# Kernel optimization log

Measured on AMD Instinct MI355X. Metric: run time of the kernel, lower is better.

Reference implementation:

```python
import jax, jax.numpy as jnp
import numpy as np


def _lstm(x, Wih, Whh, bih, bhh):
    # x: [B, T, D_in]; PyTorch gate order: i, f, g, o. Returns all hidden states [B, T, H].
    B = x.shape[0]
    H = Whh.shape[1]
    b = bih + bhh  # [4H]
    xs = jnp.transpose(x, (1, 0, 2))  # [T, B, D_in] for scan over time

    def step(carry, xt):
        h, c = carry
        gates = xt @ Wih.T + h @ Whh.T + b  # [B, 4H]
        i, f, g, o = jnp.split(gates, 4, axis=-1)
        i = jax.nn.sigmoid(i)
        f = jax.nn.sigmoid(f)
        g = jnp.tanh(g)
        o = jax.nn.sigmoid(o)
        c = f * c + i * g
        h = o * jnp.tanh(c)
        return (h, c), h

    h0 = jnp.zeros((B, H), dtype=x.dtype)
    c0 = jnp.zeros((B, H), dtype=x.dtype)
    _, hs = jax.lax.scan(step, (h0, c0), xs)  # hs: [T, B, H]
    return jnp.transpose(hs, (1, 0, 2))  # [B, T, H]


def setup_inputs() -> dict:
    key = jax.random.key(0)
    ks = jax.random.split(key, 11)
    B, T, D_IN, H1, H2, NC = 256, 2048, 16, 5, 50, 20

    def u(k, shape, fan):
        bound = 1.0 / np.sqrt(fan)
        return jax.random.uniform(k, shape, jnp.float32, -bound, bound)

    x = jax.random.normal(ks[0], (B, T, D_IN), dtype=jnp.float32)
    return {
        "x": x,
        "W1ih": u(ks[1], (4 * H1, D_IN), H1),
        "W1hh": u(ks[2], (4 * H1, H1), H1),
        "b1ih": u(ks[3], (4 * H1,), H1),
        "b1hh": u(ks[4], (4 * H1,), H1),
        "W2ih": u(ks[5], (4 * H2, H1), H2),
        "W2hh": u(ks[6], (4 * H2, H2), H2),
        "b2ih": u(ks[7], (4 * H2,), H2),
        "b2hh": u(ks[8], (4 * H2,), H2),
        "Wfc": u(ks[9], (NC, H2), H2),
        "bfc": u(ks[10], (NC,), H2),
    }


def reference(x, W1ih, W1hh, b1ih, b1hh, W2ih, W2hh, b2ih, b2hh, Wfc, bfc):
    h1 = _lstm(x, W1ih, W1hh, b1ih, b1hh)      # [B, T, 5]
    h2 = _lstm(h1, W2ih, W2hh, b2ih, b2hh)     # [B, T, 50]
    # Dropout(p=0.2) in eval mode == identity (deterministic reference)
    last = h2[:, -1, :]                        # [B, 50]
    result = last @ Wfc.T + bfc                # [B, num_classes]
    return (result, last)
```

## Files before the change

kernel.cpp:

```cpp
#include <hip/hip_runtime.h>
#include <math.h>

namespace {

constexpr int TSEQ   = 2048;
constexpr int DIN    = 16;
constexpr int NH1    = 5;
constexpr int NH2    = 50;
constexpr int NCLS   = 20;
constexpr int CHUNK  = 64;
constexpr int NCHUNK = TSEQ / CHUNK;
constexpr int BATCH  = 256;
constexpr int GSTR   = 80;
constexpr int PROW   = 4 * GSTR;

__device__ __forceinline__ float fast_sigm(float x) {
    return __fdividef(1.f, 1.f + __expf(-x));
}
__device__ __forceinline__ float fast_tanh(float x) {
    return fmaf(2.f, fast_sigm(2.f * x), -1.f);
}

template <int CTRL>
__device__ __forceinline__ float qperm(float v) {
    int i = __builtin_bit_cast(int, v);
    int r = __builtin_amdgcn_update_dpp(i, i, CTRL, 0xf, 0xf, false);
    return __builtin_bit_cast(float, r);
}
__device__ __forceinline__ float rdlane(float v, int lane) {
    return __builtin_bit_cast(float,
        __builtin_amdgcn_readlane(__builtin_bit_cast(int, v), lane));
}

#define W4_BARRIER() asm volatile("s_waitcnt lgkmcnt(0)\n\ts_barrier" ::: "memory")

template <int N> struct IC { static constexpr int v = N; };

__global__ __launch_bounds__(320, 1) void lstm_fused_kernel(
    const float* __restrict__ x,
    const float* __restrict__ W1ih,
    const float* __restrict__ W1hh,
    const float* __restrict__ b1ih,
    const float* __restrict__ b1hh,
    const float* __restrict__ W2ih,
    const float* __restrict__ W2hh,
    const float* __restrict__ b2ih,
    const float* __restrict__ b2hh,
    const float* __restrict__ Wfc,
    const float* __restrict__ bfc,
    float* __restrict__ out)
{
    const int b    = blockIdx.x;
    const int tid  = threadIdx.x;
    const int lane = tid & 63;
    const int wv   = tid >> 6;

    __shared__ __align__(16) float s_x[2][CHUNK * DIN];
    __shared__ __align__(16) float s_part[2][4][PROW];
    __shared__ __align__(16) float s_h1[2][CHUNK][8];
    __shared__ float s_h2[NH2];

    const float* xb = x + (size_t)b * TSEQ * DIN;

    if (wv == 4) {
        const int r1 = (lane < NCLS) ? ((lane & 3) * NH1 + (lane >> 2)) : 0;
        float w1h[NH1], w1x[DIN];
        #pragma unroll
        for (int j = 0; j < NH1; ++j) w1h[j] = W1hh[r1 * NH1 + j];
        #pragma unroll
        for (int d = 0; d < DIN; ++d) w1x[d] = W1ih[r1 * DIN + d];
        const float bias1 = b1ih[r1] + b1hh[r1];
        const bool  isg1  = ((lane & 3) == 2) && (lane < NCLS);
        const float isc1  = isg1 ? 2.f : 1.f;
        const float osc1  = isg1 ? 2.f : 1.f;
        const float off1  = isg1 ? -1.f : 0.f;
        float c1 = 0.f;
        float sh0v = 0.f, sh1v = 0.f, sh2v = 0.f, sh3v = 0.f, sh4v = 0.f;
        float4 xr0, xr1, xr2, xr3;

        auto l1_prod = [&](const float* xs, float* h1out) {
            float4 xv0 = *(const float4*)(xs + 0);
            float4 xv1 = *(const float4*)(xs + 4);
            float4 xv2 = *(const float4*)(xs + 8);
            float4 xv3 = *(const float4*)(xs + 12);
            float sa = fmaf(xv0.y, w1x[1],  xv0.x * w1x[0]);
            sa = fmaf(xv0.z, w1x[2], sa);  sa = fmaf(xv0.w, w1x[3], sa);
            float sb = fmaf(xv1.y, w1x[5],  xv1.x * w1x[4]);
            sb = fmaf(xv1.z, w1x[6], sb);  sb = fmaf(xv1.w, w1x[7], sb);
            float sc = fmaf(xv2.y, w1x[9],  xv2.x * w1x[8]);
            sc = fmaf(xv2.z, w1x[10], sc); sc = fmaf(xv2.w, w1x[11], sc);
            float sd = fmaf(xv3.y, w1x[13], xv3.x * w1x[12]);
            sd = fmaf(xv3.z, w1x[14], sd); sd = fmaf(xv3.w, w1x[15], sd);
            float ha = fmaf(sh1v, w1h[1], sh0v * w1h[0]);
            ha = fmaf(sh2v, w1h[2], ha);
            float hb = fmaf(sh4v, w1h[4], sh3v * w1h[3]);
            float g1 = ((sa + sb) + (sc + sd)) + ((ha + hb) + bias1);
            float act = fmaf(osc1, fast_sigm(isc1 * g1), off1);
            float f_ = qperm<0xB1>(act);
            float gg = qperm<0x4E>(act);
            float o_ = qperm<0x1B>(act);
            c1 = fmaf(f_, c1, act * gg);
            float h1me = o_ * fast_tanh(c1);
            sh0v = rdlane(h1me, 0);  sh1v = rdlane(h1me, 4);
            sh2v = rdlane(h1me, 8);  sh3v = rdlane(h1me, 12);
            sh4v = rdlane(h1me, 16);
            if ((lane & 3) == 0 && lane < NCLS) h1out[lane >> 2] = h1me;
        };

        xr0 = ((const float4*)(xb))[lane];
        xr1 = ((const float4*)(xb + 256))[lane];
        xr2 = ((const float4*)(xb + 512))[lane];
        xr3 = ((const float4*)(xb + 768))[lane];
        ((float4*)s_x[0])[lane]       = xr0;
        ((float4*)s_x[0])[64 + lane]  = xr1;
        ((float4*)s_x[0])[128 + lane] = xr2;
        ((float4*)s_x[0])[192 + lane] = xr3;
        for (int t = 0; t < CHUNK; ++t)
            l1_prod(&s_x[0][t * DIN], &s_h1[0][t][0]);
        xr0 = ((const float4*)(xb + 1024))[lane];
        xr1 = ((const float4*)(xb + 1280))[lane];
        xr2 = ((const float4*)(xb + 1536))[lane];
        xr3 = ((const float4*)(xb + 1792))[lane];
        ((float4*)s_x[1])[lane]       = xr0;
        ((float4*)s_x[1])[64 + lane]  = xr1;
        ((float4*)s_x[1])[128 + lane] = xr2;
        ((float4*)s_x[1])[192 + lane] = xr3;
        xr0 = ((const float4*)(xb + 2048))[lane];
        xr1 = ((const float4*)(xb + 2304))[lane];
        xr2 = ((const float4*)(xb + 2560))[lane];
        xr3 = ((const float4*)(xb + 2816))[lane];
        W4_BARRIER();

        #pragma unroll 1
        for (int c = 0; c < NCHUNK; ++c) {
            const int  cur   = c & 1, nxt = cur ^ 1;
            const bool w4run = (c + 1 < NCHUNK);
            if (c + 2 < NCHUNK) {
                ((float4*)s_x[cur])[lane]       = xr0;
                ((float4*)s_x[cur])[64 + lane]  = xr1;
                ((float4*)s_x[cur])[128 + lane] = xr2;
                ((float4*)s_x[cur])[192 + lane] = xr3;
                if (c + 3 < NCHUNK) {
                    const float* xc = xb + (size_t)(c + 3) * (CHUNK * DIN);
                    xr0 = ((const float4*)(xc))[lane];
                    xr1 = ((const float4*)(xc + 256))[lane];
                    xr2 = ((const float4*)(xc + 512))[lane];
                    xr3 = ((const float4*)(xc + 768))[lane];
                }
            }
            #pragma unroll 1
            for (int tt = 0; tt < CHUNK; tt += 2) {
                if (w4run) l1_prod(&s_x[nxt][tt * DIN], &s_h1[nxt][tt][0]);
                W4_BARRIER();
                if (w4run) l1_prod(&s_x[nxt][(tt + 1) * DIN], &s_h1[nxt][tt + 1][0]);
                W4_BARRIER();
            }
        }
    } else {
        auto l2loop = [&](auto cntc, auto offc) {
            constexpr int CNT = decltype(cntc)::v;
            constexpr int OFF = decltype(offc)::v;

            float wpw[4][CNT];
            #pragma unroll
            for (int i = 0; i < 4; ++i) {
                const int pr = 4 * lane + i;
                const int pg = pr >> 6;
                const int pu = pr & 63;
                #pragma unroll
                for (int kk = 0; kk < CNT; ++kk)
                    wpw[i][kk] = (pu < NH2) ? W2hh[(pg * NH2 + pu) * NH2 + (OFF + kk)]
                                            : 0.f;
            }

            const int  ul  = lane >> 2;
            const int  g   = lane & 3;
            const bool onc = (ul < CNT);
            const int  u   = OFF + (onc ? ul : 0);
            float w2i[NH1];
            float bias2 = 0.f;
            if (onc) {
                const int rr = g * NH2 + u;
                #pragma unroll
                for (int d = 0; d < NH1; ++d) w2i[d] = W2ih[rr * NH1 + d];
                bias2 = b2ih[rr] + b2hh[rr];
            } else {
                #pragma unroll
                for (int d = 0; d < NH1; ++d) w2i[d] = 0.f;
            }
            const bool  isg2 = (g == 2);
            const float isc2 = isg2 ? 2.f : 1.f;
            const float osc2 = isg2 ? 2.f : 1.f;
            const float off2 = isg2 ? -1.f : 0.f;

            float4* wpart = (float4*)(&s_part[0][wv][GSTR * (lane >> 4)]) + (lane & 15);
            const float* rpart = &s_part[0][0][g * GSTR + u];

            float hsl[CNT];
            #pragma unroll
            for (int k = 0; k < CNT; ++k) hsl[k] = 0.f;
            float c2 = 0.f;
            float4 h1a = make_float4(0.f, 0.f, 0.f, 0.f);
            float  h1e = 0.f;
            float  xp  = 0.f;

            __syncthreads();

            #pragma unroll 1
            for (int c = 0; c < NCHUNK; ++c) {
                const int cur = c & 1;

                #define L2P(BUF, TT)                                           \
                {                                                              \
                    const float* h1p = &s_h1[cur][TT][0];                      \
                    h1a = *(const float4*)h1p;       \
                    h1e = h1p[4];                                              \
                    xp = fmaf(h1a.x, w2i[0], bias2);                           \
                    xp = fmaf(h1a.y, w2i[1], xp);                              \
                    xp = fmaf(h1a.z, w2i[2], xp);                              \
                    xp = fmaf(h1a.w, w2i[3], xp);                              \
                    xp = fmaf(h1e,  w2i[4], xp);                               \
                    float a0 = 0.f, a1 = 0.f, a2 = 0.f, a3 = 0.f;              \
                    _Pragma("unroll")                                          \
                    for (int kk = 0; kk < CNT; ++kk) {                         \
                        a0 = fmaf(hsl[kk], wpw[0][kk], a0);                    \
                        a1 = fmaf(hsl[kk], wpw[1][kk], a1);                    \
                        a2 = fmaf(hsl[kk], wpw[2][kk], a2);                    \
                        a3 = fmaf(hsl[kk], wpw[3][kk], a3);                    \
                    }                                                          \
                    wpart[(BUF) * PROW] = make_float4(a0, a1, a2, a3);         \
                }

                #define L2C(BUF)                                               \
                {                                                              \
                    const float p0 = rpart[(BUF) * (4 * PROW) + 0 * PROW];     \
                    const float p1 = rpart[(BUF) * (4 * PROW) + 1 * PROW];     \
                    const float p2 = rpart[(BUF) * (4 * PROW) + 2 * PROW];     \
                    const float p3 = rpart[(BUF) * (4 * PROW) + 3 * PROW];     \
                    float pre = ((p0 + p1) + (p2 + p3)) + xp;                  \
                    float act2 = fmaf(osc2, fast_sigm(isc2 * pre), off2);      \
                    float v1 = qperm<0xB1>(act2);                              \
                    float v2 = qperm<0x4E>(act2);                              \
                    float v3 = qperm<0x1B>(act2);                              \
                    c2 = fmaf(v1, c2, act2 * v2);                              \
                    float hn = v3 * fast_tanh(c2);                             \
                    _Pragma("unroll")                                          \
                    for (int k = 0; k < CNT; ++k) hsl[k] = rdlane(hn, 4 * k);  \
                }

                #pragma unroll 1
                for (int tt = 0; tt < CHUNK; tt += 2) {
                    L2P(0, tt)
                    __syncthreads();
                    L2C(0)
                    L2P(1, tt + 1)
                    __syncthreads();
                    L2C(1)
                }
                #undef L2P
                #undef L2C
            }

            float hv = 0.f;
            #pragma unroll
            for (int j = 0; j < CNT; ++j)
                if (ul == j) hv = hsl[j];
            if (g == 0 && onc) s_h2[u] = hv;
        };

        if      (wv == 0) l2loop(IC<6>{},  IC<0>{});
        else if (wv == 1) l2loop(IC<15>{}, IC<6>{});
        else if (wv == 2) l2loop(IC<15>{}, IC<21>{});
        else              l2loop(IC<14>{}, IC<36>{});
    }

    __syncthreads();
    if (tid < NH2) out[BATCH * NCLS + b * NH2 + tid] = s_h2[tid];
    if (tid < NCLS) {
        float acc = bfc[tid];
        const float* wr = Wfc + tid * NH2;
        #pragma unroll
        for (int j = 0; j < NH2; ++j) acc = fmaf(s_h2[j], wr[j], acc);
        out[b * NCLS + tid] = acc;
    }
}

}

extern "C" void kernel_launch(void* const* d_in, const int* in_sizes, int n_in,
                              void* d_out, int out_size, void* d_ws, size_t ws_size,
                              hipStream_t stream) {
    (void)in_sizes; (void)n_in; (void)d_ws; (void)ws_size; (void)out_size;
    const float* x    = (const float*)d_in[0];
    const float* W1ih = (const float*)d_in[1];
    const float* W1hh = (const float*)d_in[2];
    const float* b1ih = (const float*)d_in[3];
    const float* b1hh = (const float*)d_in[4];
    const float* W2ih = (const float*)d_in[5];
    const float* W2hh = (const float*)d_in[6];
    const float* b2ih = (const float*)d_in[7];
    const float* b2hh = (const float*)d_in[8];
    const float* Wfc  = (const float*)d_in[9];
    const float* bfc  = (const float*)d_in[10];

    lstm_fused_kernel<<<dim3(BATCH), dim3(320), 0, stream>>>(
        x, W1ih, W1hh, b1ih, b1hh, W2ih, W2hh, b2ih, b2hh, Wfc, bfc,
        (float*)d_out);
}
```

Before: 795.2 us.

## Give each lane a full W2hh row and broadcast h2 via shared memory

Layer 2 is re-partitioned so each lane holds a complete 50-wide recurrent weight row for its own gate/unit. The split-K partial-sum exchange through shared memory is removed; each step now reads the full previous h2 vector from a double-buffered shared array. This cuts the work to one barrier per timestep, where before each step needed a partial-sum write, a barrier, a 4-way read and a readlane broadcast. The cost is more registers per lane (50 weights) and 13 vector LDS reads of h2 on every step. The layer-1 wave loop is flattened to per-timestep barriers to match.

```diff
diff --git a/kernel.cpp b/kernel.cpp
--- a/kernel.cpp
+++ b/kernel.cpp
@@ -11,8 +11,6 @@
 constexpr int CHUNK  = 64;
 constexpr int NCHUNK = TSEQ / CHUNK;
 constexpr int BATCH  = 256;
-constexpr int GSTR   = 80;
-constexpr int PROW   = 4 * GSTR;
 
 __device__ __forceinline__ float fast_sigm(float x) {
     return __fdividef(1.f, 1.f + __expf(-x));
@@ -33,8 +31,6 @@
 }
 
 #define W4_BARRIER() asm volatile("s_waitcnt lgkmcnt(0)\n\ts_barrier" ::: "memory")
-
-template <int N> struct IC { static constexpr int v = N; };
 
 __global__ __launch_bounds__(320, 1) void lstm_fused_kernel(
     const float* __restrict__ x,
@@ -56,9 +52,8 @@
     const int wv   = tid >> 6;
 
     __shared__ __align__(16) float s_x[2][CHUNK * DIN];
-    __shared__ __align__(16) float s_part[2][4][PROW];
     __shared__ __align__(16) float s_h1[2][CHUNK][8];
-    __shared__ float s_h2[NH2];
+    __shared__ __align__(16) float s_h2x[2][64];
 
     const float* xb = x + (size_t)b * TSEQ * DIN;
 
@@ -132,14 +127,14 @@
         W4_BARRIER();
 
         #pragma unroll 1
-        for (int c = 0; c < NCHUNK; ++c) {
-            const int  cur   = c & 1, nxt = cur ^ 1;
-            const bool w4run = (c + 1 < NCHUNK);
-            if (c + 2 < NCHUNK) {
-                ((float4*)s_x[cur])[lane]       = xr0;
-                ((float4*)s_x[cur])[64 + lane]  = xr1;
-                ((float4*)s_x[cur])[128 + lane] = xr2;
-                ((float4*)s_x[cur])[192 + lane] = xr3;
+        for (int t = 0; t < TSEQ; ++t) {
+            const int tt = t & (CHUNK - 1);
+            const int c  = t >> 6;
+            if (tt == 0 && c + 2 < NCHUNK) {
+                ((float4*)s_x[c & 1])[lane]       = xr0;
+                ((float4*)s_x[c & 1])[64 + lane]  = xr1;
+                ((float4*)s_x[c & 1])[128 + lane] = xr2;
+                ((float4*)s_x[c & 1])[192 + lane] = xr3;
                 if (c + 3 < NCHUNK) {
                     const float* xc = xb + (size_t)(c + 3) * (CHUNK * DIN);
                     xr0 = ((const float4*)(xc))[lane];
@@ -148,139 +143,101 @@
                     xr3 = ((const float4*)(xc + 768))[lane];
                 }
             }
-            #pragma unroll 1
-            for (int tt = 0; tt < CHUNK; tt += 2) {
-                if (w4run) l1_prod(&s_x[nxt][tt * DIN], &s_h1[nxt][tt][0]);
-                W4_BARRIER();
-                if (w4run) l1_prod(&s_x[nxt][(tt + 1) * DIN], &s_h1[nxt][tt + 1][0]);
-                W4_BARRIER();
-            }
+            if (c + 1 < NCHUNK)
+                l1_prod(&s_x[(c & 1) ^ 1][tt * DIN], &s_h1[(c & 1) ^ 1][tt][0]);
+            W4_BARRIER();
         }
     } else {
-        auto l2loop = [&](auto cntc, auto offc) {
-            constexpr int CNT = decltype(cntc)::v;
-            constexpr int OFF = decltype(offc)::v;
-
-            float wpw[4][CNT];
+        const int  ul   = lane >> 2;
+        const int  g    = lane & 3;
+        const int  uoff = (wv < 3) ? 13 * wv : 38;
+        const int  ucnt = (wv < 2) ? 13 : 12;
+        const bool on   = (ul < ucnt);
+        const int  u    = uoff + (on ? ul : 0);
+        const int  rr   = g * NH2 + u;
+
+        float w2h[NH2];
+        #pragma unroll
+        for (int k = 0; k < NH2; ++k) w2h[k] = on ? W2hh[rr * NH2 + k] : 0.f;
+        float w2i[NH1];
+        float bias2 = 0.f;
+        if (on) {
             #pragma unroll
-            for (int i = 0; i < 4; ++i) {
-                const int pr = 4 * lane + i;
-                const int pg = pr >> 6;
-                const int pu = pr & 63;
-                #pragma unroll
-                for (int kk = 0; kk < CNT; ++kk)
-                    wpw[i][kk] = (pu < NH2) ? W2hh[(pg * NH2 + pu) * NH2 + (OFF + kk)]
-                                            : 0.f;
+            for (int d = 0; d < NH1; ++d) w2i[d] = W2ih[rr * NH1 + d];
+            bias2 = b2ih[rr] + b2hh[rr];
+        } else {
+            #pragma unroll
+            for (int d = 0; d < NH1; ++d) w2i[d] = 0.f;
+        }
+        const bool  isg2 = (g == 2);
+        const float isc2 = isg2 ? 2.f : 1.f;
+        const float osc2 = isg2 ? 2.f : 1.f;
+        const float off2 = isg2 ? -1.f : 0.f;
+
+        float c2 = 0.f;
+        if (wv == 0) { s_h2x[0][lane] = 0.f; s_h2x[1][lane] = 0.f; }
+        __syncthreads();
+
+        float4 h1r4 = *(const float4*)&s_h1[0][0][0];
+        float  h1r1 = s_h1[0][0][4];
+
+        #pragma unroll 1
+        for (int t = 0; t < TSEQ; ++t) {
+            const int rsl = (t + 1) & 1;
+            const int wsl = t & 1;
+
+            const float4* hbp = (const float4*)&s_h2x[rsl][0];
+            const float4 hb0 = hbp[0],  hb1 = hbp[1],  hb2 = hbp[2];
+            const float4 hb3 = hbp[3],  hb4 = hbp[4],  hb5 = hbp[5];
+            const float4 hb6 = hbp[6],  hb7 = hbp[7],  hb8 = hbp[8];
+            const float4 hb9 = hbp[9],  hb10 = hbp[10], hb11 = hbp[11];
+            const float2 hbt = *(const float2*)&s_h2x[rsl][48];
+
+            float xq = fmaf(h1r4.x, w2i[0], bias2);
+            xq = fmaf(h1r4.y, w2i[1], xq);
+            xq = fmaf(h1r4.z, w2i[2], xq);
+            xq = fmaf(h1r4.w, w2i[3], xq);
+            xq = fmaf(h1r1,  w2i[4], xq);
+
+            {
+                const int tn = (t + 1) & (TSEQ - 1);
+                const int sl = (tn >> 6) & 1, ix = tn & (CHUNK - 1);
+                h1r4 = *(const float4*)&s_h1[sl][ix][0];
+                h1r1 = s_h1[sl][ix][4];
             }
 
-            const int  ul  = lane >> 2;
-            const int  g   = lane & 3;
-            const bool onc = (ul < CNT);
-            const int  u   = OFF + (onc ? ul : 0);
-            float w2i[NH1];
-            float bias2 = 0.f;
-            if (onc) {
-                const int rr = g * NH2 + u;
-                #pragma unroll
-                for (int d = 0; d < NH1; ++d) w2i[d] = W2ih[rr * NH1 + d];
-                bias2 = b2ih[rr] + b2hh[rr];
-            } else {
-                #pragma unroll
-                for (int d = 0; d < NH1; ++d) w2i[d] = 0.f;
-            }
-            const bool  isg2 = (g == 2);
-            const float isc2 = isg2 ? 2.f : 1.f;
-            const float osc2 = isg2 ? 2.f : 1.f;
-            const float off2 = isg2 ? -1.f : 0.f;
-
-            float4* wpart = (float4*)(&s_part[0][wv][GSTR * (lane >> 4)]) + (lane & 15);
-            const float* rpart = &s_part[0][0][g * GSTR + u];
-
-            float hsl[CNT];
-            #pragma unroll
-            for (int k = 0; k < CNT; ++k) hsl[k] = 0.f;
-            float c2 = 0.f;
-            float4 h1a = make_float4(0.f, 0.f, 0.f, 0.f);
-            float  h1e = 0.f;
-            float  xp  = 0.f;
-
+            float a0 = 0.f, a1 = 0.f, a2 = 0.f, a3 = 0.f;
+            #define HBF(J, HB)                                   \
+                a0 = fmaf(HB.x, w2h[4 * J + 0], a0);             \
+                a1 = fmaf(HB.y, w2h[4 * J + 1], a1);             \
+                a2 = fmaf(HB.z, w2h[4 * J + 2], a2);             \
+                a3 = fmaf(HB.w, w2h[4 * J + 3], a3);
+            HBF(0, hb0)  HBF(1, hb1)  HBF(2, hb2)  HBF(3, hb3)
+            HBF(4, hb4)  HBF(5, hb5)  HBF(6, hb6)  HBF(7, hb7)
+            HBF(8, hb8)  HBF(9, hb9)  HBF(10, hb10) HBF(11, hb11)
+            #undef HBF
+            a0 = fmaf(hbt.x, w2h[48], a0);
+            a1 = fmaf(hbt.y, w2h[49], a1);
+
+            float pre  = ((a0 + a1) + (a2 + a3)) + xq;
+            float act2 = fmaf(osc2, fast_sigm(isc2 * pre), off2);
+            float v1 = qperm<0xB1>(act2);
+            float v2 = qperm<0x4E>(act2);
+            float v3 = qperm<0x1B>(act2);
+            c2 = fmaf(v1, c2, act2 * v2);
+            float hn = v3 * fast_tanh(c2);
+            if (g == 0 && on) s_h2x[wsl][u] = hn;
             __syncthreads();
-
-            #pragma unroll 1
-            for (int c = 0; c < NCHUNK; ++c) {
-                const int cur = c & 1;
-
-                #define L2P(BUF, TT)                                           \
-                {                                                              \
-                    const float* h1p = &s_h1[cur][TT][0];                      \
-                    h1a = *(const float4*)h1p;       \
-                    h1e = h1p[4];                                              \
-                    xp = fmaf(h1a.x, w2i[0], bias2);                           \
-                    xp = fmaf(h1a.y, w2i[1], xp);                              \
-                    xp = fmaf(h1a.z, w2i[2], xp);                              \
-                    xp = fmaf(h1a.w, w2i[3], xp);                              \
-                    xp = fmaf(h1e,  w2i[4], xp);                               \
-                    float a0 = 0.f, a1 = 0.f, a2 = 0.f, a3 = 0.f;              \
-                    _Pragma("unroll")                                          \
-                    for (int kk = 0; kk < CNT; ++kk) {                         \
-                        a0 = fmaf(hsl[kk], wpw[0][kk], a0);                    \
-                        a1 = fmaf(hsl[kk], wpw[1][kk], a1);                    \
-                        a2 = fmaf(hsl[kk], wpw[2][kk], a2);                    \
-                        a3 = fmaf(hsl[kk], wpw[3][kk], a3);                    \
-                    }                                                          \
-                    wpart[(BUF) * PROW] = make_float4(a0, a1, a2, a3);         \
-                }
-
-                #define L2C(BUF)                                               \
-                {                                                              \
-                    const float p0 = rpart[(BUF) * (4 * PROW) + 0 * PROW];     \
-                    const float p1 = rpart[(BUF) * (4 * PROW) + 1 * PROW];     \
-                    const float p2 = rpart[(BUF) * (4 * PROW) + 2 * PROW];     \
-                    const float p3 = rpart[(BUF) * (4 * PROW) + 3 * PROW];     \
-                    float pre = ((p0 + p1) + (p2 + p3)) + xp;                  \
-                    float act2 = fmaf(osc2, fast_sigm(isc2 * pre), off2);      \
-                    float v1 = qperm<0xB1>(act2);                              \
-                    float v2 = qperm<0x4E>(act2);                              \
-                    float v3 = qperm<0x1B>(act2);                              \
-                    c2 = fmaf(v1, c2, act2 * v2);                              \
-                    float hn = v3 * fast_tanh(c2);                             \
-                    _Pragma("unroll")                                          \
-                    for (int k = 0; k < CNT; ++k) hsl[k] = rdlane(hn, 4 * k);  \
-                }
-
-                #pragma unroll 1
-                for (int tt = 0; tt < CHUNK; tt += 2) {
-                    L2P(0, tt)
-                    __syncthreads();
-                    L2C(0)
-                    L2P(1, tt + 1)
-                    __syncthreads();
-                    L2C(1)
-                }
-                #undef L2P
-                #undef L2C
-            }
-
-            float hv = 0.f;
-            #pragma unroll
-            for (int j = 0; j < CNT; ++j)
-                if (ul == j) hv = hsl[j];
-            if (g == 0 && onc) s_h2[u] = hv;
-        };
-
-        if      (wv == 0) l2loop(IC<6>{},  IC<0>{});
-        else if (wv == 1) l2loop(IC<15>{}, IC<6>{});
-        else if (wv == 2) l2loop(IC<15>{}, IC<21>{});
-        else              l2loop(IC<14>{}, IC<36>{});
+        }
     }
 
     __syncthreads();
-    if (tid < NH2) out[BATCH * NCLS + b * NH2 + tid] = s_h2[tid];
+    if (tid < NH2) out[BATCH * NCLS + b * NH2 + tid] = s_h2x[1][tid];
     if (tid < NCLS) {
         float acc = bfc[tid];
         const float* wr = Wfc + tid * NH2;
         #pragma unroll
-        for (int j = 0; j < NH2; ++j) acc = fmaf(s_h2[j], wr[j], acc);
+        for (int j = 0; j < NH2; ++j) acc = fmaf(s_h2x[1][j], wr[j], acc);
         out[b * NCLS + tid] = acc;
     }
 }
```

Result: slower. 1.290 ms (+62.2%).

## Pack two batch elements per block with 640 threads and rebalance L2 waves

Applied to the files above, without the earlier changes.

Each block now processes two batch elements, using 10 waves (4 layer-2 waves per element plus one layer-1 wave per element), and the grid is halved to 128 blocks. Shared buffers are duplicated per element, and the per-wave split of layer-2 hidden units changes from 6/15/15/14 to 10/10/15/15. The goal is to fit the 256-element batch into fewer blocks, which suits a GPU with 256 CUs, and to amortize block-wide barriers. The cost is that all 10 waves now synchronize on every step, so the slower element or wave sets the pace, and each block carries more register and LDS pressure.

```diff
diff --git a/kernel.cpp b/kernel.cpp
--- a/kernel.cpp
+++ b/kernel.cpp
@@ -36,7 +36,7 @@
 
 template <int N> struct IC { static constexpr int v = N; };
 
-__global__ __launch_bounds__(320, 1) void lstm_fused_kernel(
+__global__ __launch_bounds__(640, 1) void lstm_fused_kernel(
     const float* __restrict__ x,
     const float* __restrict__ W1ih,
     const float* __restrict__ W1hh,
@@ -50,19 +50,25 @@
     const float* __restrict__ bfc,
     float* __restrict__ out)
 {
-    const int b    = blockIdx.x;
-    const int tid  = threadIdx.x;
-    const int lane = tid & 63;
-    const int wv   = tid >> 6;
-
-    __shared__ __align__(16) float s_x[2][CHUNK * DIN];
-    __shared__ __align__(16) float s_part[2][4][PROW];
-    __shared__ __align__(16) float s_h1[2][CHUNK][8];
-    __shared__ float s_h2[NH2];
-
-    const float* xb = x + (size_t)b * TSEQ * DIN;
-
-    if (wv == 4) {
+    const int  tid  = threadIdx.x;
+    const int  lane = tid & 63;
+    const int  wv   = tid >> 6;
+    const bool isL1 = (wv >= 8);
+    const int  elem = isL1 ? (wv - 8) : (wv >> 2);
+    const int  lwv  = wv & 3;
+    const int  be   = 2 * blockIdx.x + elem;
+
+    __shared__ __align__(16) float s_x[2][2][CHUNK * DIN];
+    __shared__ __align__(16) float s_part[2][2][4][PROW];
+    __shared__ __align__(16) float s_h1[2][2][CHUNK][8];
+    __shared__ float s_h2[2][NH2];
+
+    const float* xb = x + (size_t)be * TSEQ * DIN;
+
+    if (isL1) {
+        float (*sx)[CHUNK * DIN] = s_x[elem];
+        float (*sh1)[CHUNK][8]   = s_h1[elem];
+
         const int r1 = (lane < NCLS) ? ((lane & 3) * NH1 + (lane >> 2)) : 0;
         float w1h[NH1], w1x[DIN];
         #pragma unroll
@@ -111,20 +117,20 @@
         xr1 = ((const float4*)(xb + 256))[lane];
         xr2 = ((const float4*)(xb + 512))[lane];
         xr3 = ((const float4*)(xb + 768))[lane];
-        ((float4*)s_x[0])[lane]       = xr0;
-        ((float4*)s_x[0])[64 + lane]  = xr1;
-        ((float4*)s_x[0])[128 + lane] = xr2;
-        ((float4*)s_x[0])[192 + lane] = xr3;
+        ((float4*)sx[0])[lane]       = xr0;
+        ((float4*)sx[0])[64 + lane]  = xr1;
+        ((float4*)sx[0])[128 + lane] = xr2;
+        ((float4*)sx[0])[192 + lane] = xr3;
         for (int t = 0; t < CHUNK; ++t)
-            l1_prod(&s_x[0][t * DIN], &s_h1[0][t][0]);
+            l1_prod(&sx[0][t * DIN], &sh1[0][t][0]);
         xr0 = ((const float4*)(xb + 1024))[lane];
         xr1 = ((const float4*)(xb + 1280))[lane];
         xr2 = ((const float4*)(xb + 1536))[lane];
         xr3 = ((const float4*)(xb + 1792))[lane];
-        ((float4*)s_x[1])[lane]       = xr0;
-        ((float4*)s_x[1])[64 + lane]  = xr1;
-        ((float4*)s_x[1])[128 + lane] = xr2;
-        ((float4*)s_x[1])[192 + lane] = xr3;
+        ((float4*)sx[1])[lane]       = xr0;
+        ((float4*)sx[1])[64 + lane]  = xr1;
+        ((float4*)sx[1])[128 + lane] = xr2;
+        ((float4*)sx[1])[192 + lane] = xr3;
         xr0 = ((const float4*)(xb + 2048))[lane];
         xr1 = ((const float4*)(xb + 2304))[lane];
         xr2 = ((const float4*)(xb + 2560))[lane];
@@ -136,10 +142,10 @@
             const int  cur   = c & 1, nxt = cur ^ 1;
             const bool w4run = (c + 1 < NCHUNK);
             if (c + 2 < NCHUNK) {
-                ((float4*)s_x[cur])[lane]       = xr0;
-                ((float4*)s_x[cur])[64 + lane]  = xr1;
-                ((float4*)s_x[cur])[128 + lane] = xr2;
-                ((float4*)s_x[cur])[192 + lane] = xr3;
+                ((float4*)sx[cur])[lane]       = xr0;
+                ((float4*)sx[cur])[64 + lane]  = xr1;
+                ((float4*)sx[cur])[128 + lane] = xr2;
+                ((float4*)sx[cur])[192 + lane] = xr3;
                 if (c + 3 < NCHUNK) {
                     const float* xc = xb + (size_t)(c + 3) * (CHUNK * DIN);
                     xr0 = ((const float4*)(xc))[lane];
@@ -150,13 +156,16 @@
             }
             #pragma unroll 1
             for (int tt = 0; tt < CHUNK; tt += 2) {
-                if (w4run) l1_prod(&s_x[nxt][tt * DIN], &s_h1[nxt][tt][0]);
+                if (w4run) l1_prod(&sx[nxt][tt * DIN], &sh1[nxt][tt][0]);
                 W4_BARRIER();
-                if (w4run) l1_prod(&s_x[nxt][(tt + 1) * DIN], &s_h1[nxt][tt + 1][0]);
+                if (w4run) l1_prod(&sx[nxt][(tt + 1) * DIN], &sh1[nxt][tt + 1][0]);
                 W4_BARRIER();
             }
         }
     } else {
+        float (*spart)[4][PROW] = s_part[elem];
+        float (*sh1)[CHUNK][8]  = s_h1[elem];
+
         auto l2loop = [&](auto cntc, auto offc) {
             constexpr int CNT = decltype(cntc)::v;
             constexpr int OFF = decltype(offc)::v;
@@ -193,8 +202,8 @@
             const float osc2 = isg2 ? 2.f : 1.f;
             const float off2 = isg2 ? -1.f : 0.f;
 
-            float4* wpart = (float4*)(&s_part[0][wv][GSTR * (lane >> 4)]) + (lane & 15);
-            const float* rpart = &s_part[0][0][g * GSTR + u];
+            float4* wpart = (float4*)(&spart[0][lwv][GSTR * (lane >> 4)]) + (lane & 15);
+            const float* rpart = &spart[0][0][g * GSTR + u];
 
             float hsl[CNT];
             #pragma unroll
@@ -212,7 +221,7 @@
 
                 #define L2P(BUF, TT)                                           \
                 {                                                              \
-                    const float* h1p = &s_h1[cur][TT][0];                      \
+                    const float* h1p = &sh1[cur][TT][0];                       \
                     h1a = *(const float4*)h1p;       \
                     h1e = h1p[4];                                              \
                     xp = fmaf(h1a.x, w2i[0], bias2);                           \
@@ -265,23 +274,27 @@
             #pragma unroll
             for (int j = 0; j < CNT; ++j)
                 if (ul == j) hv = hsl[j];
-            if (g == 0 && onc) s_h2[u] = hv;
+            if (g == 0 && onc) s_h2[elem][u] = hv;
         };
 
-        if      (wv == 0) l2loop(IC<6>{},  IC<0>{});
-        else if (wv == 1) l2loop(IC<15>{}, IC<6>{});
-        else if (wv == 2) l2loop(IC<15>{}, IC<21>{});
-        else              l2loop(IC<14>{}, IC<36>{});
+        if      (lwv == 0) l2loop(IC<10>{}, IC<0>{});
+        else if (lwv == 1) l2loop(IC<10>{}, IC<10>{});
+        else if (lwv == 2) l2loop(IC<15>{}, IC<20>{});
+        else               l2loop(IC<15>{}, IC<35>{});
     }
 
     __syncthreads();
-    if (tid < NH2) out[BATCH * NCLS + b * NH2 + tid] = s_h2[tid];
-    if (tid < NCLS) {
-        float acc = bfc[tid];
-        const float* wr = Wfc + tid * NH2;
-        #pragma unroll
-        for (int j = 0; j < NH2; ++j) acc = fmaf(s_h2[j], wr[j], acc);
-        out[b * NCLS + tid] = acc;
+    if (wv == 0 || wv == 4) {
+        const int e  = wv >> 2;
+        const int bo = 2 * blockIdx.x + e;
+        if (lane < NH2) out[BATCH * NCLS + bo * NH2 + lane] = s_h2[e][lane];
+        if (lane < NCLS) {
+            float acc = bfc[lane];
+            const float* wr = Wfc + lane * NH2;
+            #pragma unroll
+            for (int j = 0; j < NH2; ++j) acc = fmaf(s_h2[e][j], wr[j], acc);
+            out[bo * NCLS + lane] = acc;
+        }
     }
 }
 
@@ -303,7 +316,7 @@
     const float* Wfc  = (const float*)d_in[9];
     const float* bfc  = (const float*)d_in[10];
 
-    lstm_fused_kernel<<<dim3(BATCH), dim3(320), 0, stream>>>(
+    lstm_fused_kernel<<<dim3(BATCH / 2), dim3(640), 0, stream>>>(
         x, W1ih, W1hh, b1ih, b1hh, W2ih, W2hh, b2ih, b2hh, Wfc, bfc,
         (float*)d_out);
 }
```

Measured after the change: 1.105 ms. 1.39x slower.

## Split layer-2 LSTM across two waves with packed FMAs instead of four

Applied to the files above, without the earlier changes.

Layer 2 now runs on two wavefronts of 25 hidden units each instead of four unevenly sized waves, and the block shrinks from 320 to 192 threads. Each lane handles two units' gate updates, and the recurrent matvec uses packed two-wide FMAs (v_pk_fma_f32). The aim is to cut the partial-sum reduction from four to two reads and to make each per-step barrier cheaper with fewer waves. In exchange each wave carries more serial work and more registers per step, which lengthens the recurrent critical path.

```diff
diff --git a/kernel.cpp b/kernel.cpp
--- a/kernel.cpp
+++ b/kernel.cpp
@@ -13,6 +13,9 @@
 constexpr int BATCH  = 256;
 constexpr int GSTR   = 80;
 constexpr int PROW   = 4 * GSTR;
+constexpr int BUFF   = 2 * PROW;
+
+typedef __attribute__((ext_vector_type(2))) float f32x2;
 
 __device__ __forceinline__ float fast_sigm(float x) {
     return __fdividef(1.f, 1.f + __expf(-x));
@@ -31,12 +34,14 @@
     return __builtin_bit_cast(float,
         __builtin_amdgcn_readlane(__builtin_bit_cast(int, v), lane));
 }
+__device__ __forceinline__ f32x2 pkfma(float s, f32x2 w, f32x2 acc) {
+    f32x2 ss; ss.x = s; ss.y = s;
+    return __builtin_elementwise_fma(ss, w, acc);
+}
 
 #define W4_BARRIER() asm volatile("s_waitcnt lgkmcnt(0)\n\ts_barrier" ::: "memory")
 
-template <int N> struct IC { static constexpr int v = N; };
-
-__global__ __launch_bounds__(320, 1) void lstm_fused_kernel(
+__global__ __launch_bounds__(192, 1) void lstm_fused_kernel(
     const float* __restrict__ x,
     const float* __restrict__ W1ih,
     const float* __restrict__ W1hh,
@@ -56,13 +61,13 @@
     const int wv   = tid >> 6;
 
     __shared__ __align__(16) float s_x[2][CHUNK * DIN];
-    __shared__ __align__(16) float s_part[2][4][PROW];
+    __shared__ __align__(16) float s_part[2][2][PROW];
     __shared__ __align__(16) float s_h1[2][CHUNK][8];
     __shared__ float s_h2[NH2];
 
     const float* xb = x + (size_t)b * TSEQ * DIN;
 
-    if (wv == 4) {
+    if (wv == 2) {
         const int r1 = (lane < NCLS) ? ((lane & 3) * NH1 + (lane >> 2)) : 0;
         float w1h[NH1], w1x[DIN];
         #pragma unroll
@@ -156,125 +161,131 @@
                 W4_BARRIER();
             }
         }
+        __syncthreads();
     } else {
-        auto l2loop = [&](auto cntc, auto offc) {
-            constexpr int CNT = decltype(cntc)::v;
-            constexpr int OFF = decltype(offc)::v;
-
-            float wpw[4][CNT];
-            #pragma unroll
-            for (int i = 0; i < 4; ++i) {
-                const int pr = 4 * lane + i;
-                const int pg = pr >> 6;
-                const int pu = pr & 63;
-                #pragma unroll
-                for (int kk = 0; kk < CNT; ++kk)
-                    wpw[i][kk] = (pu < NH2) ? W2hh[(pg * NH2 + pu) * NH2 + (OFF + kk)]
-                                            : 0.f;
-            }
-
-            const int  ul  = lane >> 2;
-            const int  g   = lane & 3;
-            const bool onc = (ul < CNT);
-            const int  u   = OFF + (onc ? ul : 0);
-            float w2i[NH1];
-            float bias2 = 0.f;
-            if (onc) {
-                const int rr = g * NH2 + u;
-                #pragma unroll
-                for (int d = 0; d < NH1; ++d) w2i[d] = W2ih[rr * NH1 + d];
-                bias2 = b2ih[rr] + b2hh[rr];
-            } else {
-                #pragma unroll
-                for (int d = 0; d < NH1; ++d) w2i[d] = 0.f;
-            }
-            const bool  isg2 = (g == 2);
-            const float isc2 = isg2 ? 2.f : 1.f;
-            const float osc2 = isg2 ? 2.f : 1.f;
-            const float off2 = isg2 ? -1.f : 0.f;
-
-            float4* wpart = (float4*)(&s_part[0][wv][GSTR * (lane >> 4)]) + (lane & 15);
-            const float* rpart = &s_part[0][0][g * GSTR + u];
-
-            float hsl[CNT];
-            #pragma unroll
-            for (int k = 0; k < CNT; ++k) hsl[k] = 0.f;
-            float c2 = 0.f;
-            float4 h1a = make_float4(0.f, 0.f, 0.f, 0.f);
-            float  h1e = 0.f;
-            float  xp  = 0.f;
-
-            __syncthreads();
+        const int OFF = 25 * wv;
+
+        const int pr0 = 4 * lane;
+        const int pg  = pr0 >> 6;
+        const int pu0 = pr0 & 63;
+        f32x2 wp01[25], wp23[25];
+        #pragma unroll
+        for (int kk = 0; kk < 25; ++kk) {
+            const int k = OFF + kk;
+            wp01[kk].x = (pu0 + 0 < NH2) ? W2hh[(pg * NH2 + pu0 + 0) * NH2 + k] : 0.f;
+            wp01[kk].y = (pu0 + 1 < NH2) ? W2hh[(pg * NH2 + pu0 + 1) * NH2 + k] : 0.f;
+            wp23[kk].x = (pu0 + 2 < NH2) ? W2hh[(pg * NH2 + pu0 + 2) * NH2 + k] : 0.f;
+            wp23[kk].y = (pu0 + 3 < NH2) ? W2hh[(pg * NH2 + pu0 + 3) * NH2 + k] : 0.f;
+        }
+
+        const int  ul   = lane >> 2;
+        const int  g    = lane & 3;
+        const int  u1   = OFF + ul;
+        const bool has2 = (ul < 9);
+        const int  u2   = OFF + 16 + (has2 ? ul : 0);
+        const int  rr1  = g * NH2 + u1;
+        const int  rr2  = g * NH2 + u2;
+        f32x2 w2i12[NH1], b2;
+        #pragma unroll
+        for (int d = 0; d < NH1; ++d) {
+            w2i12[d].x = W2ih[rr1 * NH1 + d];
+            w2i12[d].y = has2 ? W2ih[rr2 * NH1 + d] : 0.f;
+        }
+        b2.x = b2ih[rr1] + b2hh[rr1];
+        b2.y = has2 ? (b2ih[rr2] + b2hh[rr2]) : 0.f;
+        const bool  isg2 = (g == 2);
+        const float isc2 = isg2 ? 2.f : 1.f;
+        const float osc2 = isg2 ? 2.f : 1.f;
+        const float off2 = isg2 ? -1.f : 0.f;
+
+        float4* wpart = (float4*)(&s_part[0][wv][GSTR * (lane >> 4)]) + (lane & 15);
+        const float* rpart = &s_part[0][0][g * GSTR + u1];
+
+        float hsl[25];
+        #pragma unroll
+        for (int k = 0; k < 25; ++k) hsl[k] = 0.f;
+        float c2a = 0.f, c2b = 0.f;
+        float4 h1a = make_float4(0.f, 0.f, 0.f, 0.f);
+        float  h1e = 0.f;
+        f32x2  xp12; xp12.x = 0.f; xp12.y = 0.f;
+
+        __syncthreads();
+
+        #pragma unroll 1
+        for (int c = 0; c < NCHUNK; ++c) {
+            const int cur = c & 1;
+
+            #define L2P(BUF, TT)                                           \
+            {                                                              \
+                const float* h1p = &s_h1[cur][TT][0];                      \
+                h1a = *(const float4*)h1p;       \
+                h1e = h1p[4];                                              \
+                xp12 = b2;                                                 \
+                xp12 = pkfma(h1a.x, w2i12[0], xp12);                       \
+                xp12 = pkfma(h1a.y, w2i12[1], xp12);                       \
+                xp12 = pkfma(h1a.z, w2i12[2], xp12);                       \
+                xp12 = pkfma(h1a.w, w2i12[3], xp12);                       \
+                xp12 = pkfma(h1e,  w2i12[4], xp12);                        \
+                f32x2 a01; a01.x = 0.f; a01.y = 0.f;                       \
+                f32x2 a23; a23.x = 0.f; a23.y = 0.f;                       \
+                _Pragma("unroll")                                          \
+                for (int kk = 0; kk < 25; ++kk) {                          \
+                    a01 = pkfma(hsl[kk], wp01[kk], a01);                   \
+                    a23 = pkfma(hsl[kk], wp23[kk], a23);                   \
+                }                                                          \
+                wpart[(BUF) * (BUFF / 4)] = make_float4(a01.x, a01.y,      \
+                                                        a23.x, a23.y);     \
+            }
+
+            #define L2C(BUF)                                               \
+            {                                                              \
+                const float* rb = rpart + (BUF) * BUFF;                    \
+                const float p0 = rb[0];                                    \
+                const float p1 = rb[PROW];                                 \
+                const float q0 = rb[16];                                   \
+                const float q1 = rb[PROW + 16];                            \
+                float pre1 = (p0 + p1) + xp12.x;                           \
+                float pre2 = (q0 + q1) + xp12.y;                           \
+                float act1 = fmaf(osc2, fast_sigm(isc2 * pre1), off2);     \
+                float act2 = fmaf(osc2, fast_sigm(isc2 * pre2), off2);     \
+                float f1 = qperm<0xB1>(act1);                              \
+                float g1 = qperm<0x4E>(act1);                              \
+                float o1 = qperm<0x1B>(act1);                              \
+                float f2 = qperm<0xB1>(act2);                              \
+                float g2 = qperm<0x4E>(act2);                              \
+                float o2 = qperm<0x1B>(act2);                              \
+                c2a = fmaf(f1, c2a, act1 * g1);                            \
+                c2b = fmaf(f2, c2b, act2 * g2);                            \
+                float hn1 = o1 * fast_tanh(c2a);                           \
+                float hn2 = o2 * fast_tanh(c2b);                           \
+                _Pragma("unroll")                                          \
+                for (int k = 0; k < 16; ++k) hsl[k] = rdlane(hn1, 4 * k);  \
+                _Pragma("unroll")                                          \
+                for (int k = 0; k < 9; ++k)                                \
+                    hsl[16 + k] = rdlane(hn2, 4 * k);                      \
+            }
 
             #pragma unroll 1
-            for (int c = 0; c < NCHUNK; ++c) {
-                const int cur = c & 1;
-
-                #define L2P(BUF, TT)                                           \
-                {                                                              \
-                    const float* h1p = &s_h1[cur][TT][0];                      \
-                    h1a = *(const float4*)h1p;       \
-                    h1e = h1p[4];                                              \
-                    xp = fmaf(h1a.x, w2i[0], bias2);                           \
-                    xp = fmaf(h1a.y, w2i[1], xp);                              \
-                    xp = fmaf(h1a.z, w2i[2], xp);                              \
-                    xp = fmaf(h1a.w, w2i[3], xp);                              \
-                    xp = fmaf(h1e,  w2i[4], xp);                               \
-                    float a0 = 0.f, a1 = 0.f, a2 = 0.f, a3 = 0.f;              \
-                    _Pragma("unroll")                                          \
-                    for (int kk = 0; kk < CNT; ++kk) {                         \
-                        a0 = fmaf(hsl[kk], wpw[0][kk], a0);                    \
-                        a1 = fmaf(hsl[kk], wpw[1][kk], a1);                    \
-                        a2 = fmaf(hsl[kk], wpw[2][kk], a2);                    \
-                        a3 = fmaf(hsl[kk], wpw[3][kk], a3);                    \
-                    }                                                          \
-                    wpart[(BUF) * PROW] = make_float4(a0, a1, a2, a3);         \
-                }
-
-                #define L2C(BUF)                                               \
-                {                                                              \
-                    const float p0 = rpart[(BUF) * (4 * PROW) + 0 * PROW];     \
-                    const float p1 = rpart[(BUF) * (4 * PROW) + 1 * PROW];     \
-                    const float p2 = rpart[(BUF) * (4 * PROW) + 2 * PROW];     \
-                    const float p3 = rpart[(BUF) * (4 * PROW) + 3 * PROW];     \
-                    float pre = ((p0 + p1) + (p2 + p3)) + xp;                  \
-                    float act2 = fmaf(osc2, fast_sigm(isc2 * pre), off2);      \
-                    float v1 = qperm<0xB1>(act2);                              \
-                    float v2 = qperm<0x4E>(act2);                              \
-                    float v3 = qperm<0x1B>(act2);                              \
-                    c2 = fmaf(v1, c2, act2 * v2);                              \
-                    float hn = v3 * fast_tanh(c2);                             \
-                    _Pragma("unroll")                                          \
-                    for (int k = 0; k < CNT; ++k) hsl[k] = rdlane(hn, 4 * k);  \
-                }
-
-                #pragma unroll 1
-                for (int tt = 0; tt < CHUNK; tt += 2) {
-                    L2P(0, tt)
-                    __syncthreads();
-                    L2C(0)
-                    L2P(1, tt + 1)
-                    __syncthreads();
-                    L2C(1)
-                }
-                #undef L2P
-                #undef L2C
-            }
-
-            float hv = 0.f;
-            #pragma unroll
-            for (int j = 0; j < CNT; ++j)
-                if (ul == j) hv = hsl[j];
-            if (g == 0 && onc) s_h2[u] = hv;
-        };
-
-        if      (wv == 0) l2loop(IC<6>{},  IC<0>{});
-        else if (wv == 1) l2loop(IC<15>{}, IC<6>{});
-        else if (wv == 2) l2loop(IC<15>{}, IC<21>{});
-        else              l2loop(IC<14>{}, IC<36>{});
+            for (int tt = 0; tt < CHUNK; tt += 2) {
+                L2P(0, tt)
+                __syncthreads();
+                L2C(0)
+                L2P(1, tt + 1)
+                __syncthreads();
+                L2C(1)
+            }
+            #undef L2P
+            #undef L2C
+        }
+
+        float hv = 0.f;
+        #pragma unroll
+        for (int j = 0; j < 25; ++j)
+            if (lane == j) hv = hsl[j];
+        if (lane < 25) s_h2[OFF + lane] = hv;
+        __syncthreads();
     }
 
-    __syncthreads();
     if (tid < NH2) out[BATCH * NCLS + b * NH2 + tid] = s_h2[tid];
     if (tid < NCLS) {
         float acc = bfc[tid];
@@ -303,7 +314,7 @@
     const float* Wfc  = (const float*)d_in[9];
     const float* bfc  = (const float*)d_in[10];
 
-    lstm_fused_kernel<<<dim3(BATCH), dim3(320), 0, stream>>>(
+    lstm_fused_kernel<<<dim3(BATCH), dim3(192), 0, stream>>>(
         x, W1ih, W1hh, b1ih, b1hh, W2ih, W2hh, b2ih, b2hh, Wfc, bfc,
         (float*)d_out);
 }
```

After: 952.7 us. 19.8% more time.
